# Kernel optimization log

Measured on AMD Instinct MI355X. Metric: run time of the kernel, lower is better.

The kernel has to match this reference:

```python
import jax, jax.numpy as jnp
import numpy as np

MARGIN = 1.0


def setup_inputs() -> dict:
    key = jax.random.key(0)
    k1, k2, k3, k4 = jax.random.split(key, 4)
    B, C, D = 8192, 100, 128
    z = jax.random.normal(k1, (B, C, D), dtype=jnp.float32)
    kernel_weight = jax.random.normal(k2, (C, D), dtype=jnp.float32)
    o = jax.random.normal(k3, (B, C), dtype=jnp.float32)
    y = jax.random.randint(k4, (B,), 0, C, dtype=jnp.int64)
    return {"z": z, "kernel_weight": kernel_weight, "o": o, "y": y}


def reference(z, kernel_weight, o, y):
    B, C, D = z.shape
    # classification loss: MSE(o, one_hot(y))
    y_one_hot = jax.nn.one_hot(y, C, dtype=o.dtype)  # [B, C]
    loss_cls = jnp.mean((o - y_one_hot) ** 2)

    # clustering-close: sum_c mean((z[y==c, c, :] - w[c])^2)
    # = sum_c segsum_c(||z[i, y_i] - w[y_i]||^2) / (count_c * D)
    z_own = z[jnp.arange(B), y]            # [B, D] gather of each sample's own-class slice
    diff = z_own - kernel_weight[y]        # [B, D]
    per_sample = jnp.sum(diff * diff, axis=-1)  # [B]
    sums = jax.ops.segment_sum(per_sample, y, num_segments=C)       # [C]
    counts = jax.ops.segment_sum(jnp.ones_like(per_sample), y, num_segments=C)  # [C]
    loss_close = jnp.sum(sums / (counts * D))

    # clustering-dist: sum_c relu(margin - MSE(w[j!=c], stop_grad(w[c]))) / C
    w_sg = jax.lax.stop_gradient(kernel_weight)
    pd = jnp.sum((kernel_weight[None, :, :] - w_sg[:, None, :]) ** 2, axis=-1)  # [C, C]; diag is 0
    S = jnp.sum(pd, axis=1) / ((C - 1) * D)  # [C] per-class MSE to other centers
    loss_dist = jnp.sum(jnp.maximum(MARGIN - S, 0.0)) / C

    total = loss_cls + loss_close + loss_dist
    return (total, loss_cls, loss_close, loss_dist)
```

## Files before the change

kernel.cpp:

```cpp
#include <hip/hip_runtime.h>

#define MARGIN 1.0f
#define BB  8192
#define CC  100
#define DD  128
#define NBM 256
#define TPB 512

__device__ __forceinline__ float wave_reduce_sum(float v) {
    #pragma unroll
    for (int off = 32; off > 0; off >>= 1)
        v += __shfl_down(v, off, 64);
    return v;
}

__device__ __forceinline__ float block_reduce_sum(float v, float* s8) {
    int lane = threadIdx.x & 63, wid = threadIdx.x >> 6;
    v = wave_reduce_sum(v);
    if (lane == 0) s8[wid] = v;
    __syncthreads();
    float r = 0.f;
    if (wid == 0) {
        r = (lane < (TPB / 64)) ? s8[lane] : 0.f;
        r = wave_reduce_sum(r);
    }
    __syncthreads();
    return r;
}

__global__ void __launch_bounds__(TPB) k1_main(
        const float* __restrict__ z, const float* __restrict__ w,
        const float* __restrict__ o, const int* __restrict__ y,
        float* __restrict__ ws) {
    const int t = threadIdx.x;
    const int blk = blockIdx.x;

    if (blk == NBM) {
        __shared__ float s8[TPB / 64];
        __shared__ float s_vec[DD];
        __shared__ float s_p[TPB];
        __shared__ float s_bc;
        int d = t & 127, qq = t >> 7;
        float a = 0.f;
        for (int j = qq; j < CC; j += 4) a += w[j * DD + d];
        s_p[t] = a;
        __syncthreads();
        if (t < 128) s_vec[t] = s_p[t] + s_p[t + 128] + s_p[t + 256] + s_p[t + 384];
        __syncthreads();

        float norm_i = 0.f, dot_i = 0.f;
        if (t < CC) {
            const float4* wp = reinterpret_cast<const float4*>(w + (size_t)t * DD);
            #pragma unroll 8
            for (int k = 0; k < DD / 4; ++k) {
                float4 v = wp[k];
                norm_i += v.x*v.x + v.y*v.y + v.z*v.z + v.w*v.w;
                dot_i  += v.x*s_vec[4*k] + v.y*s_vec[4*k+1]
                        + v.z*s_vec[4*k+2] + v.w*s_vec[4*k+3];
            }
        }
        float sumNorm = block_reduce_sum((t < CC) ? norm_i : 0.f, s8);
        if (t == 0) s_bc = sumNorm;
        __syncthreads();
        sumNorm = s_bc;

        float contrib = 0.f;
        if (t < CC) {
            float S = (sumNorm + (float)CC * norm_i - 2.f * dot_i)
                      / ((float)(CC - 1) * (float)DD);
            contrib = fmaxf(MARGIN - S, 0.f) / (float)CC;
        }
        contrib = block_reduce_sum(contrib, s8);
        if (t == 0) ws[2 * NBM] = contrib;
        return;
    }

    const int lane16 = t & 15;
    const int s = blk * (TPB / 16) + (t >> 4);
    int yb = y[s];

    const float4* zp = reinterpret_cast<const float4*>(z + ((size_t)s * CC + yb) * DD);
    const float4* wp = reinterpret_cast<const float4*>(w + (size_t)yb * DD);
    float4 a0 = zp[lane16];
    float4 a1 = zp[lane16 + 16];
    float4 b0 = wp[lane16];
    float4 b1 = wp[lane16 + 16];

    const float4* o4 = reinterpret_cast<const float4*>(o);
    const int nq = BB * CC / 4;
    const int qi  = blk * TPB + t;
    const int qi2 = qi + NBM * TPB;
    float4 ov0 = o4[qi];
    const bool has2 = (qi2 < nq);
    float4 ov1 = has2 ? o4[qi2] : make_float4(0.f, 0.f, 0.f, 0.f);

    const int4* y4 = reinterpret_cast<const int4*>(y);
    int4 r0 = y4[t];
    int4 r1 = y4[t + 512];
    int4 r2 = y4[t + 1024];
    int4 r3 = y4[t + 1536];

    __shared__ int hist[128];
    if (t < 128) hist[t] = 0;
    __syncthreads();
    atomicAdd(&hist[r0.x], 1); atomicAdd(&hist[r0.y], 1);
    atomicAdd(&hist[r0.z], 1); atomicAdd(&hist[r0.w], 1);
    atomicAdd(&hist[r1.x], 1); atomicAdd(&hist[r1.y], 1);
    atomicAdd(&hist[r1.z], 1); atomicAdd(&hist[r1.w], 1);
    atomicAdd(&hist[r2.x], 1); atomicAdd(&hist[r2.y], 1);
    atomicAdd(&hist[r2.z], 1); atomicAdd(&hist[r2.w], 1);
    atomicAdd(&hist[r3.x], 1); atomicAdd(&hist[r3.y], 1);
    atomicAdd(&hist[r3.z], 1); atomicAdd(&hist[r3.w], 1);
    __syncthreads();

    const int perRow = CC / 4;
    float clsAcc;
    {
        int b  = qi / perRow;
        int c0 = (qi - b * perRow) * 4;
        int yv = y[b];
        float e0 = ov0.x - ((c0 + 0 == yv) ? 1.f : 0.f);
        float e1 = ov0.y - ((c0 + 1 == yv) ? 1.f : 0.f);
        float e2 = ov0.z - ((c0 + 2 == yv) ? 1.f : 0.f);
        float e3 = ov0.w - ((c0 + 3 == yv) ? 1.f : 0.f);
        clsAcc = e0*e0 + e1*e1 + e2*e2 + e3*e3;
    }
    if (has2) {
        int b  = qi2 / perRow;
        int c0 = (qi2 - b * perRow) * 4;
        int yv = y[b];
        float e0 = ov1.x - ((c0 + 0 == yv) ? 1.f : 0.f);
        float e1 = ov1.y - ((c0 + 1 == yv) ? 1.f : 0.f);
        float e2 = ov1.z - ((c0 + 2 == yv) ? 1.f : 0.f);
        float e3 = ov1.w - ((c0 + 3 == yv) ? 1.f : 0.f);
        clsAcc += e0*e0 + e1*e1 + e2*e2 + e3*e3;
    }

    float e0 = a0.x-b0.x, e1 = a0.y-b0.y, e2 = a0.z-b0.z, e3 = a0.w-b0.w;
    float f0 = a1.x-b1.x, f1 = a1.y-b1.y, f2 = a1.z-b1.z, f3 = a1.w-b1.w;
    float v = e0*e0 + e1*e1 + e2*e2 + e3*e3
            + f0*f0 + f1*f1 + f2*f2 + f3*f3;
    v += __shfl_xor(v, 1, 64);
    v += __shfl_xor(v, 2, 64);
    v += __shfl_xor(v, 4, 64);
    v += __shfl_xor(v, 8, 64);
    float closeAcc = 0.f;
    if (lane16 == 0)
        closeAcc = v / ((float)hist[yb] * (float)DD);

    const int lane = t & 63, wid = t >> 6;
    float v0 = closeAcc, v1 = clsAcc;
    #pragma unroll
    for (int off = 32; off > 0; off >>= 1) {
        v0 += __shfl_down(v0, off, 64);
        v1 += __shfl_down(v1, off, 64);
    }
    __shared__ float sc[TPB / 64], sk[TPB / 64];
    if (lane == 0) { sc[wid] = v0; sk[wid] = v1; }
    __syncthreads();
    if (t == 0) {
        float c = 0.f, k = 0.f;
        #pragma unroll
        for (int i = 0; i < TPB / 64; ++i) { c += sc[i]; k += sk[i]; }
        ws[blk] = c;
        ws[NBM + blk] = k;
    }
}

__global__ void __launch_bounds__(64) k2_final(const float* __restrict__ ws,
                                               float* __restrict__ out) {
    int lane = threadIdx.x;
    const float4* p = reinterpret_cast<const float4*>(ws);
    float4 a = p[lane];
    float4 b = p[64 + lane];
    float c = a.x + a.y + a.z + a.w;
    float k = b.x + b.y + b.z + b.w;
    #pragma unroll
    for (int off = 32; off > 0; off >>= 1) {
        c += __shfl_down(c, off, 64);
        k += __shfl_down(k, off, 64);
    }
    if (lane == 0) {
        float cls  = k / ((float)BB * (float)CC);
        float dist = ws[2 * NBM];
        out[0] = cls + c + dist;
        out[1] = cls;
        out[2] = c;
        out[3] = dist;
    }
}

extern "C" void kernel_launch(void* const* d_in, const int* in_sizes, int n_in,
                              void* d_out, int out_size, void* d_ws, size_t ws_size,
                              hipStream_t stream) {
    const float* z = (const float*)d_in[0];
    const float* w = (const float*)d_in[1];
    const float* o = (const float*)d_in[2];
    const int*   y = (const int*)d_in[3];
    float* out = (float*)d_out;
    float* ws  = (float*)d_ws;

    k1_main<<<NBM + 1, TPB, 0, stream>>>(z, w, o, y, ws);
    k2_final<<<1, 64, 0, stream>>>(ws, out);
}
```

Baseline: 13.51 us.

## Fuse final reduction into main kernel via last-block atomic counter

Replaces the separate finalisation kernel with a last-block-done pattern. Each block publishes its partials with atomics and a fence, then bumps a global counter, and whichever block sees the final count reduces all partials and writes the outputs. This removes one kernel launch and its gap. In exchange it adds a memset of the counter before the launch plus fence and atomic overhead.

```diff
diff --git a/kernel.cpp b/kernel.cpp
--- a/kernel.cpp
+++ b/kernel.cpp
@@ -6,6 +6,7 @@
 #define DD  128
 #define NBM 256
 #define TPB 512
+
 
 __device__ __forceinline__ float wave_reduce_sum(float v) {
     #pragma unroll
@@ -28,12 +29,14 @@
     return r;
 }
 
-__global__ void __launch_bounds__(TPB) k1_main(
+__global__ void __launch_bounds__(TPB) fused(
         const float* __restrict__ z, const float* __restrict__ w,
         const float* __restrict__ o, const int* __restrict__ y,
-        float* __restrict__ ws) {
+        float* __restrict__ ws, float* __restrict__ out) {
     const int t = threadIdx.x;
     const int blk = blockIdx.x;
+    int* ctr = reinterpret_cast<int*>(ws + 2 * NBM + 1);
+    __shared__ int s_old;
 
     if (blk == NBM) {
         __shared__ float s8[TPB / 64];
@@ -71,122 +74,128 @@
             contrib = fmaxf(MARGIN - S, 0.f) / (float)CC;
         }
         contrib = block_reduce_sum(contrib, s8);
-        if (t == 0) ws[2 * NBM] = contrib;
-        return;
+        if (t == 0) {
+            atomicExch(&ws[2 * NBM], contrib);
+            __threadfence();
+            s_old = atomicAdd(ctr, 1);
+        }
+    } else {
+        const int lane16 = t & 15;
+        const int s = blk * (TPB / 16) + (t >> 4);
+        int yb = y[s];
+
+        const float4* zp = reinterpret_cast<const float4*>(z + ((size_t)s * CC + yb) * DD);
+        const float4* wp = reinterpret_cast<const float4*>(w + (size_t)yb * DD);
+        float4 a0 = zp[lane16];
+        float4 a1 = zp[lane16 + 16];
+        float4 b0 = wp[lane16];
+        float4 b1 = wp[lane16 + 16];
+
+        const float4* o4 = reinterpret_cast<const float4*>(o);
+        const int nq = BB * CC / 4;
+        const int qi  = blk * TPB + t;
+        const int qi2 = qi + NBM * TPB;
+        float4 ov0 = o4[qi];
+        const bool has2 = (qi2 < nq);
+        float4 ov1 = has2 ? o4[qi2] : make_float4(0.f, 0.f, 0.f, 0.f);
+
+        const int4* y4 = reinterpret_cast<const int4*>(y);
+        int4 r0 = y4[t];
+        int4 r1 = y4[t + 512];
+        int4 r2 = y4[t + 1024];
+        int4 r3 = y4[t + 1536];
+
+        __shared__ int hist[128];
+        if (t < 128) hist[t] = 0;
+        __syncthreads();
+        atomicAdd(&hist[r0.x], 1); atomicAdd(&hist[r0.y], 1);
+        atomicAdd(&hist[r0.z], 1); atomicAdd(&hist[r0.w], 1);
+        atomicAdd(&hist[r1.x], 1); atomicAdd(&hist[r1.y], 1);
+        atomicAdd(&hist[r1.z], 1); atomicAdd(&hist[r1.w], 1);
+        atomicAdd(&hist[r2.x], 1); atomicAdd(&hist[r2.y], 1);
+        atomicAdd(&hist[r2.z], 1); atomicAdd(&hist[r2.w], 1);
+        atomicAdd(&hist[r3.x], 1); atomicAdd(&hist[r3.y], 1);
+        atomicAdd(&hist[r3.z], 1); atomicAdd(&hist[r3.w], 1);
+        __syncthreads();
+
+        const int perRow = CC / 4;
+        float clsAcc;
+        {
+            int b  = qi / perRow;
+            int c0 = (qi - b * perRow) * 4;
+            int yv = y[b];
+            float e0 = ov0.x - ((c0 + 0 == yv) ? 1.f : 0.f);
+            float e1 = ov0.y - ((c0 + 1 == yv) ? 1.f : 0.f);
+            float e2 = ov0.z - ((c0 + 2 == yv) ? 1.f : 0.f);
+            float e3 = ov0.w - ((c0 + 3 == yv) ? 1.f : 0.f);
+            clsAcc = e0*e0 + e1*e1 + e2*e2 + e3*e3;
+        }
+        if (has2) {
+            int b  = qi2 / perRow;
+            int c0 = (qi2 - b * perRow) * 4;
+            int yv = y[b];
+            float e0 = ov1.x - ((c0 + 0 == yv) ? 1.f : 0.f);
+            float e1 = ov1.y - ((c0 + 1 == yv) ? 1.f : 0.f);
+            float e2 = ov1.z - ((c0 + 2 == yv) ? 1.f : 0.f);
+            float e3 = ov1.w - ((c0 + 3 == yv) ? 1.f : 0.f);
+            clsAcc += e0*e0 + e1*e1 + e2*e2 + e3*e3;
+        }
+
+        float e0 = a0.x-b0.x, e1 = a0.y-b0.y, e2 = a0.z-b0.z, e3 = a0.w-b0.w;
+        float f0 = a1.x-b1.x, f1 = a1.y-b1.y, f2 = a1.z-b1.z, f3 = a1.w-b1.w;
+        float v = e0*e0 + e1*e1 + e2*e2 + e3*e3
+                + f0*f0 + f1*f1 + f2*f2 + f3*f3;
+        v += __shfl_xor(v, 1, 64);
+        v += __shfl_xor(v, 2, 64);
+        v += __shfl_xor(v, 4, 64);
+        v += __shfl_xor(v, 8, 64);
+        float closeAcc = 0.f;
+        if (lane16 == 0)
+            closeAcc = v / ((float)hist[yb] * (float)DD);
+
+        const int lane = t & 63, wid = t >> 6;
+        float v0 = closeAcc, v1 = clsAcc;
+        #pragma unroll
+        for (int off = 32; off > 0; off >>= 1) {
+            v0 += __shfl_down(v0, off, 64);
+            v1 += __shfl_down(v1, off, 64);
+        }
+        __shared__ float sc[TPB / 64], sk[TPB / 64];
+        if (lane == 0) { sc[wid] = v0; sk[wid] = v1; }
+        __syncthreads();
+        if (t == 0) {
+            float c = 0.f, k = 0.f;
+            #pragma unroll
+            for (int i = 0; i < TPB / 64; ++i) { c += sc[i]; k += sk[i]; }
+            atomicExch(&ws[blk], c);
+            atomicExch(&ws[NBM + blk], k);
+            __threadfence();
+            s_old = atomicAdd(ctr, 1);
+        }
     }
 
-    const int lane16 = t & 15;
-    const int s = blk * (TPB / 16) + (t >> 4);
-    int yb = y[s];
-
-    const float4* zp = reinterpret_cast<const float4*>(z + ((size_t)s * CC + yb) * DD);
-    const float4* wp = reinterpret_cast<const float4*>(w + (size_t)yb * DD);
-    float4 a0 = zp[lane16];
-    float4 a1 = zp[lane16 + 16];
-    float4 b0 = wp[lane16];
-    float4 b1 = wp[lane16 + 16];
-
-    const float4* o4 = reinterpret_cast<const float4*>(o);
-    const int nq = BB * CC / 4;
-    const int qi  = blk * TPB + t;
-    const int qi2 = qi + NBM * TPB;
-    float4 ov0 = o4[qi];
-    const bool has2 = (qi2 < nq);
-    float4 ov1 = has2 ? o4[qi2] : make_float4(0.f, 0.f, 0.f, 0.f);
-
-    const int4* y4 = reinterpret_cast<const int4*>(y);
-    int4 r0 = y4[t];
-    int4 r1 = y4[t + 512];
-    int4 r2 = y4[t + 1024];
-    int4 r3 = y4[t + 1536];
-
-    __shared__ int hist[128];
-    if (t < 128) hist[t] = 0;
     __syncthreads();
-    atomicAdd(&hist[r0.x], 1); atomicAdd(&hist[r0.y], 1);
-    atomicAdd(&hist[r0.z], 1); atomicAdd(&hist[r0.w], 1);
-    atomicAdd(&hist[r1.x], 1); atomicAdd(&hist[r1.y], 1);
-    atomicAdd(&hist[r1.z], 1); atomicAdd(&hist[r1.w], 1);
-    atomicAdd(&hist[r2.x], 1); atomicAdd(&hist[r2.y], 1);
-    atomicAdd(&hist[r2.z], 1); atomicAdd(&hist[r2.w], 1);
-    atomicAdd(&hist[r3.x], 1); atomicAdd(&hist[r3.y], 1);
-    atomicAdd(&hist[r3.z], 1); atomicAdd(&hist[r3.w], 1);
-    __syncthreads();
-
-    const int perRow = CC / 4;
-    float clsAcc;
-    {
-        int b  = qi / perRow;
-        int c0 = (qi - b * perRow) * 4;
-        int yv = y[b];
-        float e0 = ov0.x - ((c0 + 0 == yv) ? 1.f : 0.f);
-        float e1 = ov0.y - ((c0 + 1 == yv) ? 1.f : 0.f);
-        float e2 = ov0.z - ((c0 + 2 == yv) ? 1.f : 0.f);
-        float e3 = ov0.w - ((c0 + 3 == yv) ? 1.f : 0.f);
-        clsAcc = e0*e0 + e1*e1 + e2*e2 + e3*e3;
-    }
-    if (has2) {
-        int b  = qi2 / perRow;
-        int c0 = (qi2 - b * perRow) * 4;
-        int yv = y[b];
-        float e0 = ov1.x - ((c0 + 0 == yv) ? 1.f : 0.f);
-        float e1 = ov1.y - ((c0 + 1 == yv) ? 1.f : 0.f);
-        float e2 = ov1.z - ((c0 + 2 == yv) ? 1.f : 0.f);
-        float e3 = ov1.w - ((c0 + 3 == yv) ? 1.f : 0.f);
-        clsAcc += e0*e0 + e1*e1 + e2*e2 + e3*e3;
-    }
-
-    float e0 = a0.x-b0.x, e1 = a0.y-b0.y, e2 = a0.z-b0.z, e3 = a0.w-b0.w;
-    float f0 = a1.x-b1.x, f1 = a1.y-b1.y, f2 = a1.z-b1.z, f3 = a1.w-b1.w;
-    float v = e0*e0 + e1*e1 + e2*e2 + e3*e3
-            + f0*f0 + f1*f1 + f2*f2 + f3*f3;
-    v += __shfl_xor(v, 1, 64);
-    v += __shfl_xor(v, 2, 64);
-    v += __shfl_xor(v, 4, 64);
-    v += __shfl_xor(v, 8, 64);
-    float closeAcc = 0.f;
-    if (lane16 == 0)
-        closeAcc = v / ((float)hist[yb] * (float)DD);
-
-    const int lane = t & 63, wid = t >> 6;
-    float v0 = closeAcc, v1 = clsAcc;
-    #pragma unroll
-    for (int off = 32; off > 0; off >>= 1) {
-        v0 += __shfl_down(v0, off, 64);
-        v1 += __shfl_down(v1, off, 64);
-    }
-    __shared__ float sc[TPB / 64], sk[TPB / 64];
-    if (lane == 0) { sc[wid] = v0; sk[wid] = v1; }
-    __syncthreads();
-    if (t == 0) {
+    if (s_old == NBM && t < 64) {
+        __threadfence();
         float c = 0.f, k = 0.f;
         #pragma unroll
-        for (int i = 0; i < TPB / 64; ++i) { c += sc[i]; k += sk[i]; }
-        ws[blk] = c;
-        ws[NBM + blk] = k;
-    }
-}
-
-__global__ void __launch_bounds__(64) k2_final(const float* __restrict__ ws,
-                                               float* __restrict__ out) {
-    int lane = threadIdx.x;
-    const float4* p = reinterpret_cast<const float4*>(ws);
-    float4 a = p[lane];
-    float4 b = p[64 + lane];
-    float c = a.x + a.y + a.z + a.w;
-    float k = b.x + b.y + b.z + b.w;
-    #pragma unroll
-    for (int off = 32; off > 0; off >>= 1) {
-        c += __shfl_down(c, off, 64);
-        k += __shfl_down(k, off, 64);
-    }
-    if (lane == 0) {
-        float cls  = k / ((float)BB * (float)CC);
-        float dist = ws[2 * NBM];
-        out[0] = cls + c + dist;
-        out[1] = cls;
-        out[2] = c;
-        out[3] = dist;
+        for (int i = 0; i < NBM / 64; ++i) {
+            c += atomicAdd(&ws[i * 64 + t], 0.f);
+            k += atomicAdd(&ws[NBM + i * 64 + t], 0.f);
+        }
+        #pragma unroll
+        for (int off = 32; off > 0; off >>= 1) {
+            c += __shfl_down(c, off, 64);
+            k += __shfl_down(k, off, 64);
+        }
+        if (t == 0) {
+            float cls  = k / ((float)BB * (float)CC);
+            float dist = atomicAdd(&ws[2 * NBM], 0.f);
+            out[0] = cls + c + dist;
+            out[1] = cls;
+            out[2] = c;
+            out[3] = dist;
+        }
     }
 }
 
@@ -200,6 +209,6 @@
     float* out = (float*)d_out;
     float* ws  = (float*)d_ws;
 
-    k1_main<<<NBM + 1, TPB, 0, stream>>>(z, w, o, y, ws);
-    k2_final<<<1, 64, 0, stream>>>(ws, out);
-}
+    hipMemsetAsync((char*)d_ws + (2 * NBM + 1) * sizeof(float), 0, sizeof(int), stream);
+    fused<<<NBM + 1, TPB, 0, stream>>>(z, w, o, y, ws, out);
+}
```

After: 22.40 us. +65.8%, slower.
